# Optimization experiments

Hardware: AMD Instinct MI355X
Metric: run time of the kernel (lower is better)

Reference implementation:

```python
import jax, jax.numpy as jnp
import numpy as np

HEAD = 8

def _mvn(x, eps=1e-5):
    # per-(batch,channel) mean/std over spatial dims; torch .var default is unbiased (ddof=1)
    mean = jnp.mean(x, axis=(2, 3), keepdims=True)
    var = jnp.var(x, axis=(2, 3), ddof=1, keepdims=True) + eps
    return (x - mean) / jnp.sqrt(var)

def _conv1x1(x, w, b):
    return jnp.einsum('bchw,oc->bohw', x, w) + b[None, :, None, None]

def _block_heads(x, p):
    # non-overlapping unfold (kernel==stride==p): pure reshape; matches torch unfold ordering
    b, c, h, w = x.shape
    y = x.reshape(b, c, h // p, p, w // p, p).transpose(0, 1, 2, 4, 3, 5)
    n, r = (h // p) * (w // p), p * p
    return y.reshape(b, HEAD, c // HEAD, n, r)

def _unblock(x, p, h, w):
    # inverse of non-overlapping unfold (fold with kernel==stride)
    b, c, n, r = x.shape
    y = x.reshape(b, c, h // p, w // p, p, p).transpose(0, 1, 2, 4, 3, 5)
    return y.reshape(b, c, h, w)

def setup_inputs() -> dict:
    key = jax.random.key(0)
    ks = jax.random.split(key, 12)
    B, C, H, W = 4, 512, 64, 64
    wmat = lambda k: jax.random.normal(k, (C, C), jnp.float32) * 0.05
    zb = jnp.zeros((C,), jnp.float32)
    return {
        'content': jax.random.normal(ks[0], (B, C, H, W), jnp.float32),
        'style': jax.random.normal(ks[1], (B, C, H, W), jnp.float32),
        'q_w': wmat(ks[2]), 'q_b': zb,
        'k_w': wmat(ks[3]), 'k_b': zb,
        'v_w': wmat(ks[4]), 'v_b': zb,
        'q2_w': wmat(ks[5]), 'q2_b': zb,
        'k2_w': wmat(ks[6]), 'k2_b': zb,
        'v2_w': wmat(ks[7]), 'v2_b': zb,
        'f1_w': wmat(ks[8]), 'f1_b': zb,
        'f2_w': wmat(ks[9]), 'f2_b': zb,
        'sim_alpha': jnp.ones((1,), jnp.float32),
        'sim_beta': jnp.zeros((1,), jnp.float32),
        'layer': 3,
    }

def reference(content, style, q_w, q_b, k_w, k_b, v_w, v_b, q2_w, q2_b, k2_w, k2_b,
              v2_w, v2_b, f1_w, f1_b, f2_w, f2_b, sim_alpha, sim_beta, layer):
    region = 8 if int(layer) in (3, 4) else 4
    b, c, h, w = content.shape
    nc = _mvn(content)
    ns = _mvn(style)
    DA_q = _block_heads(_conv1x1(nc, q_w, q_b), region)      # [b,H,ch,n,r]
    DA_k = _block_heads(_conv1x1(ns, k_w, k_b), region)
    DA_v = _block_heads(_conv1x1(style, v_w, v_b), region)
    PA_q = _block_heads(_conv1x1(nc, q2_w, q2_b), region)
    PA_k = _block_heads(_conv1x1(ns, k2_w, k2_b), region)
    PA_v = _block_heads(_conv1x1(style, v2_w, v2_b), region)
    r = region * region
    n = DA_q.shape[3]
    # --- distinctiveness attention: mean-center clustering + sigmoid-weighted aggregation ---
    DA_k_c = jnp.mean(DA_k, axis=-1)                          # [b,H,ch,n]
    DA_v_c = jnp.mean(DA_v, axis=-1)
    dis = jnp.einsum('bhcx,bhcxy->bhxy', DA_k_c, DA_k)
    sim = jax.nn.sigmoid(sim_beta + sim_alpha * dis)          # [b,H,n,r]
    DA_k_agg = (jnp.einsum('bhxy,bhcxy->bhcx', sim, DA_k) + DA_k_c) / (r + 1)
    DA_v_agg = (jnp.einsum('bhxy,bhcxy->bhcx', sim, DA_v) + DA_v_c) / (r + 1)
    logits = jnp.einsum('bhcxy,bhcz->bhyxz', DA_q, DA_k_agg)  # [b,H,r,n,n]
    scores = jax.nn.softmax(logits, axis=-1)
    DA = jnp.einsum('bhyxz,bhcz->bhcxy', scores, DA_v_agg)    # [b,H,ch,n,r]
    DA_ub = _unblock(DA.reshape(b, c, n, r), region, h, w)
    # --- point attention: argmax NN block matching, then intra-block attention ---
    PA1 = jnp.einsum('bhcxy,bhczy->bhxz', PA_q, PA_k)         # [b,H,n,n]
    idx = jnp.argmax(PA1, axis=-1)                            # [b,H,n]
    idx_b = jnp.broadcast_to(idx[:, :, None, :, None], PA_k.shape)
    PA_k_rs = jnp.take_along_axis(PA_k, idx_b, axis=3)
    PA_v_rs = jnp.take_along_axis(PA_v, idx_b, axis=3)
    logits2 = jnp.einsum('bhcxy,bhcxz->bhxyz', PA_q, PA_k_rs) # [b,H,n,r,r]
    scores2 = jax.nn.softmax(logits2, axis=-1)
    PA = jnp.einsum('bhxyz,bhcxz->bhcxy', scores2, PA_v_rs)
    PA_ub = _unblock(PA.reshape(b, c, n, r), region, h, w)
    O = _conv1x1(DA_ub, f1_w, f1_b) + _conv1x1(PA_ub, f2_w, f2_b)
    return O + content
```

## Files before the change

kernel.cpp:

```cpp
#include <hip/hip_runtime.h>

typedef unsigned short u16;
typedef unsigned int   u32;
typedef _Float16       f16;

typedef f16   f16x8 __attribute__((ext_vector_type(8)));
typedef f16   f16x4 __attribute__((ext_vector_type(4)));
typedef float f32x4 __attribute__((ext_vector_type(4)));

__device__ __forceinline__ f32x4 mfma16(f16x8 a, f16x8 b, f32x4 c){
  return __builtin_amdgcn_mfma_f32_16x16x32_f16(a, b, c, 0, 0, 0);
}

__device__ __forceinline__ void glds16(const f16* g, f16* l){
  __builtin_amdgcn_global_load_lds(
      (const __attribute__((address_space(1))) void*)g,
      (__attribute__((address_space(3))) void*)l, 16, 0, 0);
}

__device__ __forceinline__ void barrier_f(){
  __builtin_amdgcn_s_barrier();
  asm volatile("" ::: "memory");
}

__global__ __launch_bounds__(256) void k_mvn_stats(
    const float* __restrict__ content, const float* __restrict__ style,
    float* __restrict__ stats)
{
  const int src = blockIdx.x >> 11;
  const int row = blockIdx.x & 2047;
  const float* xp = (src ? style : content) + (size_t)row * 4096;
  const int t = threadIdx.x;
  double s = 0.0, ss = 0.0;
  for(int i = t * 4; i < 4096; i += 1024){
    float4 v = *(const float4*)(xp + i);
    s  += (double)v.x + (double)v.y + (double)v.z + (double)v.w;
    ss += (double)v.x * v.x + (double)v.y * v.y + (double)v.z * v.z + (double)v.w * v.w;
  }
  #pragma unroll
  for(int off = 32; off > 0; off >>= 1){
    s  += __shfl_xor(s, off);
    ss += __shfl_xor(ss, off);
  }
  __shared__ double sh[8];
  const int wid = t >> 6;
  if((t & 63) == 0){ sh[wid] = s; sh[4 + wid] = ss; }
  __syncthreads();
  if(t == 0){
    double S  = sh[0] + sh[1] + sh[2] + sh[3];
    double SS = sh[4] + sh[5] + sh[6] + sh[7];
    float mean = (float)(S * (1.0 / 4096.0));
    float var  = (float)((SS - S * S * (1.0 / 4096.0)) * (1.0 / 4095.0));
    stats[src * 4096 + row] = mean;
    stats[src * 4096 + 2048 + row] = rsqrtf(var + 1e-5f);
  }
}

__global__ __launch_bounds__(256) void k_prep_w_all(
    const float* __restrict__ qW,  const float* __restrict__ qB,
    const float* __restrict__ kW,  const float* __restrict__ kB,
    const float* __restrict__ q2W, const float* __restrict__ q2B,
    const float* __restrict__ k2W, const float* __restrict__ k2B,
    const float* __restrict__ vW,  const float* __restrict__ vB,
    const float* __restrict__ v2W, const float* __restrict__ v2B,
    const float* __restrict__ f1W, const float* __restrict__ f2W,
    const float* __restrict__ stats,
    f16* __restrict__ qw, f16* __restrict__ kw,
    f16* __restrict__ q2wh, f16* __restrict__ q2wl,
    f16* __restrict__ k2wh, f16* __restrict__ k2wl,
    f16* __restrict__ vw, f16* __restrict__ v2w,
    f16* __restrict__ f1w, f16* __restrict__ f2w,
    float* __restrict__ biasp)
{
  const int t = threadIdx.x;
  int rid = blockIdx.x * 32 + (t >> 3);
  const float *W; const float *B = nullptr;
  int side = -1, b = 0, o;
  f16 *oh; f16 *ol = nullptr; float* bs = nullptr;
  if(rid < 2048){
    b = rid >> 9; o = rid & 511;
    W = qW; B = qB; side = 0;
    oh = qw + (size_t)(b * 512 + o) * 512;
    bs = biasp + 0 * 2048 + b * 512 + o;
  } else if(rid < 4096){
    rid -= 2048; b = rid >> 9; o = rid & 511;
    W = kW; B = kB; side = 1;
    oh = kw + (size_t)(b * 512 + o) * 512;
    bs = biasp + 1 * 2048 + b * 512 + o;
  } else if(rid < 6144){
    rid -= 4096; b = rid >> 9; o = rid & 511;
    W = q2W; B = q2B; side = 0;
    oh = q2wh + (size_t)(b * 512 + o) * 512;
    ol = q2wl + (size_t)(b * 512 + o) * 512;
    bs = biasp + 4 * 2048 + b * 512 + o;
  } else if(rid < 8192){
    rid -= 6144; b = rid >> 9; o = rid & 511;
    W = k2W; B = k2B; side = 1;
    oh = k2wh + (size_t)(b * 512 + o) * 512;
    ol = k2wl + (size_t)(b * 512 + o) * 512;
    bs = biasp + 5 * 2048 + b * 512 + o;
  } else if(rid < 8704){
    o = rid - 8192; W = vW; B = vB;
    oh = vw + (size_t)o * 512;
    bs = biasp + 2 * 2048 + o;
  } else if(rid < 9216){
    o = rid - 8704; W = v2W; B = v2B;
    oh = v2w + (size_t)o * 512;
    bs = biasp + 3 * 2048 + o;
  } else if(rid < 9728){
    o = rid - 9216; W = f1W;
    oh = f1w + (size_t)o * 512;
  } else {
    o = rid - 9728; W = f2W;
    oh = f2w + (size_t)o * 512;
  }
  const float* mp = (side >= 0) ? stats + side * 4096 + b * 512 : nullptr;
  const float* rp = (side >= 0) ? mp + 2048 : nullptr;
  const int c0 = (t & 7) * 64;
  float dot = 0.f;
  #pragma unroll
  for(int i = 0; i < 64; i += 8){
    int c = c0 + i;
    float w[8];
    *(float4*)(w)     = *(const float4*)(W + (size_t)o * 512 + c);
    *(float4*)(w + 4) = *(const float4*)(W + (size_t)o * 512 + c + 4);
    f16x8 h8, l8;
    #pragma unroll
    for(int j = 0; j < 8; j++){
      float wp = w[j];
      if(side >= 0){
        float r = rp[c + j];
        dot += wp * mp[c + j] * r;
        wp *= r;
      }
      f16 h = (f16)wp;
      h8[j] = h; l8[j] = (f16)(wp - (float)h);
    }
    *(f16x8*)(oh + c) = h8;
    if(ol) *(f16x8*)(ol + c) = l8;
  }
  if(bs){
    dot += __shfl_xor(dot, 1); dot += __shfl_xor(dot, 2); dot += __shfl_xor(dot, 4);
    if((t & 7) == 0) *bs = B[o] - dot;
  }
}

__global__ __launch_bounds__(256) void k_prep_x(
    const float* __restrict__ content, const float* __restrict__ style,
    f16* __restrict__ cth, f16* __restrict__ ctl,
    f16* __restrict__ sth, f16* __restrict__ stl)
{
  const int side = blockIdx.z;
  const int b = blockIdx.y;
  const int s0 = blockIdx.x * 128;
  const float* Xb = (side ? style : content) + (size_t)b * 512 * 4096;
  f16* Oh = (side ? sth : cth) + (size_t)b * 4096 * 512;
  f16* Ol = (side ? stl : ctl) + (size_t)b * 4096 * 512;
  __shared__ float Xs[32][132];
  const int t = threadIdx.x;
  const int s = t >> 1, half = t & 1;
  for(int cc = 0; cc < 512; cc += 32){
    __syncthreads();
    #pragma unroll
    for(int u = 0; u < 4; u++){
      int q = t + u * 256;
      int row = q >> 5, f4 = q & 31;
      float4 v = *(const float4*)(Xb + (size_t)(cc + row) * 4096 + s0 + f4 * 4);
      *(float4*)(&Xs[row][f4 * 4]) = v;
    }
    __syncthreads();
    f16x8 h0, h1, l0, l1;
    #pragma unroll
    for(int i = 0; i < 8; i++){
      float x = Xs[half * 16 + i][s];
      f16 h = (f16)x; h0[i] = h; l0[i] = (f16)(x - (float)h);
    }
    #pragma unroll
    for(int i = 0; i < 8; i++){
      float x = Xs[half * 16 + 8 + i][s];
      f16 h = (f16)x; h1[i] = h; l1[i] = (f16)(x - (float)h);
    }
    size_t o = (size_t)(s0 + s) * 512 + cc + half * 16;
    *(f16x8*)(Oh + o) = h0; *(f16x8*)(Oh + o + 8) = h1;
    *(f16x8*)(Ol + o) = l0; *(f16x8*)(Ol + o + 8) = l1;
  }
}

__global__ __launch_bounds__(256) void k_convT(
    const f16* __restrict__ Xt, const f16* __restrict__ Wp,
    const float* __restrict__ bias, int bw, f16* __restrict__ Out)
{
  const int b = blockIdx.z;
  const int o0 = blockIdx.y * 128;
  const int s0 = blockIdx.x * 128;
  const f16* Xb = Xt + (size_t)b * 4096 * 512;
  const f16* Wb = Wp + (bw ? (size_t)b * 262144 : 0);
  const float* bp = bias + (bw ? b * 512 : 0);
  f16* Ob = Out + (size_t)b * 512 * 4096;
  __shared__ f16 As[2][4096];
  __shared__ f16 Bs[2][4096];
  const int t = threadIdx.x;
  const int lane = t & 63, wid = t >> 6;
  const int wm = (wid >> 1) * 64, wn = (wid & 1) * 64;
  const int lr = lane & 15, lg = lane >> 4;
  const int sr = lane >> 2, sc = lane & 3;
  auto STAGE = [&](int d, int kk){
    #pragma unroll
    for(int i = 0; i < 2; i++){
      int r0 = wid * 32 + i * 16;
      int rr = r0 + sr;
      int cs = (sc ^ ((rr >> 1) & 3)) << 3;
      glds16(Wb + (size_t)(o0 + rr) * 512 + kk + cs, As[d] + r0 * 32);
      glds16(Xb + (size_t)(s0 + rr) * 512 + kk + cs, Bs[d] + r0 * 32);
    }
  };
  f32x4 acc[4][4] = {};
  STAGE(0, 0);
  int db = 0;
  for(int tt = 0; tt < 16; tt++){
    if(tt < 15){
      STAGE(db ^ 1, (tt + 1) * 32);
      asm volatile("s_waitcnt vmcnt(4)" ::: "memory");
    } else {
      asm volatile("s_waitcnt vmcnt(0)" ::: "memory");
    }
    barrier_f();
    f16x8 av[4], bv[4];
    #pragma unroll
    for(int mi = 0; mi < 4; mi++){
      int row = wm + mi * 16 + lr;
      av[mi] = *(const f16x8*)(As[db] + row * 32 + ((lg ^ ((row >> 1) & 3)) << 3));
    }
    #pragma unroll
    for(int ni = 0; ni < 4; ni++){
      int row = wn + ni * 16 + lr;
      bv[ni] = *(const f16x8*)(Bs[db] + row * 32 + ((lg ^ ((row >> 1) & 3)) << 3));
    }
    #pragma unroll
    for(int mi = 0; mi < 4; mi++){
      #pragma unroll
      for(int ni = 0; ni < 4; ni++)
        acc[mi][ni] = mfma16(av[mi], bv[ni], acc[mi][ni]);
    }
    barrier_f();
    db ^= 1;
  }
  #pragma unroll
  for(int mi = 0; mi < 4; mi++){
    #pragma unroll
    for(int ni = 0; ni < 4; ni++){
      #pragma unroll
      for(int j = 0; j < 4; j++){
        int o = o0 + wm + mi * 16 + lg * 4 + j;
        int s = s0 + wn + ni * 16 + lr;
        Ob[(size_t)o * 4096 + s] = (f16)(acc[mi][ni][j] + bp[o]);
      }
    }
  }
}

__global__ __launch_bounds__(256) void k_conv3out(
    const f16* __restrict__ Xt,
    const f16* __restrict__ Wk, const f16* __restrict__ Wv, const f16* __restrict__ Wv2,
    const float* __restrict__ biasp,
    f16* __restrict__ Ok, f16* __restrict__ Ov, f16* __restrict__ Ov2)
{
  const int b = blockIdx.z;
  const int seg = blockIdx.y >> 2;
  const int o0 = (blockIdx.y & 3) * 128;
  const int s0 = blockIdx.x * 128;
  const f16* Xb = Xt + (size_t)b * 4096 * 512;
  const f16* Wb = seg == 0 ? Wk + (size_t)b * 262144 : (seg == 1 ? Wv : Wv2);
  const float* bp = biasp + (seg == 0 ? 1 * 2048 + b * 512 : (seg == 1 ? 2 * 2048 : 3 * 2048));
  f16* Ob = (seg == 0 ? Ok : (seg == 1 ? Ov : Ov2)) + (size_t)b * 512 * 4096;
  __shared__ f16 As[2][4096];
  __shared__ f16 Bs[2][4096];
  const int t = threadIdx.x;
  const int lane = t & 63, wid = t >> 6;
  const int wm = (wid >> 1) * 64, wn = (wid & 1) * 64;
  const int lr = lane & 15, lg = lane >> 4;
  const int sr = lane >> 2, sc = lane & 3;
  auto STAGE = [&](int d, int kk){
    #pragma unroll
    for(int i = 0; i < 2; i++){
      int r0 = wid * 32 + i * 16;
      int rr = r0 + sr;
      int cs = (sc ^ ((rr >> 1) & 3)) << 3;
      glds16(Wb + (size_t)(o0 + rr) * 512 + kk + cs, As[d] + r0 * 32);
      glds16(Xb + (size_t)(s0 + rr) * 512 + kk + cs, Bs[d] + r0 * 32);
    }
  };
  f32x4 acc[4][4] = {};
  STAGE(0, 0);
  int db = 0;
  for(int tt = 0; tt < 16; tt++){
    if(tt < 15){
      STAGE(db ^ 1, (tt + 1) * 32);
      asm volatile("s_waitcnt vmcnt(4)" ::: "memory");
    } else {
      asm volatile("s_waitcnt vmcnt(0)" ::: "memory");
    }
    barrier_f();
    f16x8 av[4], bv[4];
    #pragma unroll
    for(int mi = 0; mi < 4; mi++){
      int row = wm + mi * 16 + lr;
      av[mi] = *(const f16x8*)(As[db] + row * 32 + ((lg ^ ((row >> 1) & 3)) << 3));
    }
    #pragma unroll
    for(int ni = 0; ni < 4; ni++){
      int row = wn + ni * 16 + lr;
      bv[ni] = *(const f16x8*)(Bs[db] + row * 32 + ((lg ^ ((row >> 1) & 3)) << 3));
    }
    #pragma unroll
    for(int mi = 0; mi < 4; mi++){
      #pragma unroll
      for(int ni = 0; ni < 4; ni++)
        acc[mi][ni] = mfma16(av[mi], bv[ni], acc[mi][ni]);
    }
    barrier_f();
    db ^= 1;
  }
  #pragma unroll
  for(int mi = 0; mi < 4; mi++){
    #pragma unroll
    for(int ni = 0; ni < 4; ni++){
      #pragma unroll
      for(int j = 0; j < 4; j++){
        int o = o0 + wm + mi * 16 + lg * 4 + j;
        int s = s0 + wn + ni * 16 + lr;
        Ob[(size_t)o * 4096 + s] = (f16)(acc[mi][ni][j] + bp[o]);
      }
    }
  }
}

__global__ __launch_bounds__(256) void k_pa1(
    const f16* __restrict__ Qh, const f16* __restrict__ Kh, float* __restrict__ pa1p)
{
  const int slice = blockIdx.x & 7;
  const int bh = blockIdx.x >> 3;
  const size_t base = (size_t)bh * 64 * 4096;
  __shared__ f16 Ah[2][64][72], Bh[2][64][72];
  const int t = threadIdx.x;
  const int lane = t & 63, wid = t >> 6;
  const int wm = (wid >> 1) * 32, wn = (wid & 1) * 32;
  const int lr = lane & 15, lg = lane >> 4;
  f32x4 acc[2][2] = {};
  for(int chunk = 0; chunk < 4; chunk++){
    const int c0 = slice * 8 + chunk * 2;
    __syncthreads();
    #pragma unroll
    for(int cc = 0; cc < 2; cc++){
      size_t cbase = base + (size_t)(c0 + cc) * 4096;
      #pragma unroll
      for(int u = 0; u < 2; u++){
        int e = u * 256 + t;
        int x = e >> 3, yh = e & 7;
        size_t src = cbase + (size_t)((x >> 3) * 512 + (x & 7) * 8 + yh * 64);
        int dst = yh * 8;
        *(f16x8*)(&Ah[cc][x][dst]) = *(const f16x8*)(Qh + src);
        *(f16x8*)(&Bh[cc][x][dst]) = *(const f16x8*)(Kh + src);
      }
    }
    __syncthreads();
    #pragma unroll
    for(int cc = 0; cc < 2; cc++){
      #pragma unroll
      for(int kc = 0; kc < 2; kc++){
        f16x8 ah[2], bh[2];
        #pragma unroll
        for(int mi = 0; mi < 2; mi++)
          ah[mi] = *(const f16x8*)(&Ah[cc][wm + mi * 16 + lr][kc * 32 + lg * 8]);
        #pragma unroll
        for(int ni = 0; ni < 2; ni++)
          bh[ni] = *(const f16x8*)(&Bh[cc][wn + ni * 16 + lr][kc * 32 + lg * 8]);
        #pragma unroll
        for(int mi = 0; mi < 2; mi++){
          #pragma unroll
          for(int ni = 0; ni < 2; ni++)
            acc[mi][ni] = mfma16(ah[mi], bh[ni], acc[mi][ni]);
        }
      }
    }
  }
  float* outp = pa1p + ((size_t)bh * 8 + slice) * 4096;
  #pragma unroll
  for(int mi = 0; mi < 2; mi++){
    #pragma unroll
    for(int ni = 0; ni < 2; ni++){
      #pragma unroll
      for(int j = 0; j < 4; j++){
        int x = wm + mi * 16 + lg * 4 + j;
        int z = wn + ni * 16 + lr;
        outp[x * 64 + z] = acc[mi][ni][j];
      }
    }
  }
}

__global__ __launch_bounds__(64) void k_pa1r(
    float* __restrict__ pa1p, int* __restrict__ idx, int* __restrict__ flags)
{
  const int bh = blockIdx.x;
  const int x = threadIdx.x;
  float* p = pa1p + (size_t)bh * 8 * 4096 + x * 64;
  float m1 = -3e38f, m2 = -3e38f; int i1 = 0;
  for(int z = 0; z < 64; z += 4){
    float4 v = *(const float4*)(p + z);
    #pragma unroll
    for(int sl = 1; sl < 8; sl++){
      float4 w = *(const float4*)(p + sl * 4096 + z);
      v.x += w.x; v.y += w.y; v.z += w.z; v.w += w.w;
    }
    *(float4*)(p + z) = v;
    float vv[4] = {v.x, v.y, v.z, v.w};
    #pragma unroll
    for(int k = 0; k < 4; k++){
      if(vv[k] > m1){ m2 = m1; m1 = vv[k]; i1 = z + k; }
      else if(vv[k] > m2){ m2 = vv[k]; }
    }
  }
  idx[bh * 64 + x] = i1;
  flags[bh * 64 + x] = (m2 >= m1 - 0.5f) ? 1 : 0;
}

__global__ __launch_bounds__(256) void k_refine(
    const f16* __restrict__ Xqh, const f16* __restrict__ Xql,
    const f16* __restrict__ Xkh, const f16* __restrict__ Xkl,
    const f16* __restrict__ Wqh, const f16* __restrict__ Wql,
    const f16* __restrict__ Wkh, const f16* __restrict__ Wkl,
    const float* __restrict__ biasp, const float* __restrict__ pa1p,
    const int* __restrict__ flags, int* __restrict__ idx)
{
  const int bid = blockIdx.x;
  if(flags[bid] == 0) return;
  const int bh = bid >> 6, x = bid & 63;
  const int b = bh >> 3, hd = bh & 7;
  __shared__ __align__(16) f16 Ah[64][72], Al[64][72], Bh[64][72], Bl[64][72];
  __shared__ float q2s[64][65];
  __shared__ float red[4];
  __shared__ float vals[64];
  __shared__ int cand[64];
  const int t = threadIdx.x;
  const int lane = t & 63, wid = t >> 6;
  const int wm = (wid >> 1) * 32, wn = (wid & 1) * 32;
  const int lr = lane & 15, lg = lane >> 4;
  const int srw = t >> 2, soc = (t & 3) * 2;

  auto gemm = [&](const f16* Wh_, const f16* Wl_, const f16* Xh_, const f16* Xl_,
                  int blk, f32x4 (&acc)[2][2]){
    const size_t wrow = ((size_t)(b * 512 + hd * 64 + srw)) * 512 + soc * 8;
    const int s = (blk >> 3) * 512 + (blk & 7) * 8 + (srw >> 3) * 64 + (srw & 7);
    const size_t xrow = ((size_t)b * 4096 + s) * 512 + soc * 8;
    f16x8 r0, r1, r2, r3, r4, r5, r6, r7;
    #define RLOAD(ch, a0,a1,a2,a3,a4,a5,a6,a7) do{            \
      a0 = *(const f16x8*)(Wh_ + wrow + (ch) * 64);           \
      a1 = *(const f16x8*)(Wh_ + wrow + (ch) * 64 + 8);       \
      a2 = *(const f16x8*)(Wl_ + wrow + (ch) * 64);           \
      a3 = *(const f16x8*)(Wl_ + wrow + (ch) * 64 + 8);       \
      a4 = *(const f16x8*)(Xh_ + xrow + (ch) * 64);           \
      a5 = *(const f16x8*)(Xh_ + xrow + (ch) * 64 + 8);       \
      a6 = *(const f16x8*)(Xl_ + xrow + (ch) * 64);           \
      a7 = *(const f16x8*)(Xl_ + xrow + (ch) * 64 + 8);       \
    }while(0)
    RLOAD(0, r0,r1,r2,r3,r4,r5,r6,r7);
    #pragma unroll
    for(int ch = 0; ch < 8; ch++){
      __syncthreads();
      *(f16x8*)(&Ah[srw][soc * 8])     = r0;
      *(f16x8*)(&Ah[srw][soc * 8 + 8]) = r1;
      *(f16x8*)(&Al[srw][soc * 8])     = r2;
      *(f16x8*)(&Al[srw][soc * 8 + 8]) = r3;
      *(f16x8*)(&Bh[srw][soc * 8])     = r4;
      *(f16x8*)(&Bh[srw][soc * 8 + 8]) = r5;
      *(f16x8*)(&Bl[srw][soc * 8])     = r6;
      *(f16x8*)(&Bl[srw][soc * 8 + 8]) = r7;
      f16x8 n0, n1, n2, n3, n4, n5, n6, n7;
      if(ch < 7) RLOAD(ch + 1, n0,n1,n2,n3,n4,n5,n6,n7);
// ... 283 lines not shown
    }
  }
}

__global__ __launch_bounds__(256) void k_pa2(
    const f16* __restrict__ Qh, const f16* __restrict__ Kh,
    const f16* __restrict__ V2, const int* __restrict__ idx, f16* __restrict__ OutT)
{
  const int hw = blockIdx.x;
  const int bh = (hw & 7) * 4 + ((hw >> 3) >> 6);
  const int x  = (hw >> 3) & 63;
  const int b_ = bh >> 3, hd = bh & 7;
  const size_t base = (size_t)bh * 64 * 4096;
  f16* Ot = OutT + (size_t)b_ * 4096 * 512 + hd * 64;

  __shared__ __align__(16) char Ubuf[18432];
  __shared__ f16 Vn[64][72];
  __shared__ f16 Ps[64][72];
  f16   (*Qt)[72] = (f16(*)[72])Ubuf;
  f16   (*Kt)[72] = (f16(*)[72])(Ubuf + 9216);
  float (*Lf)[66] = (float(*)[66])Ubuf;
  float (*Os)[67] = (float(*)[67])Ubuf;

  const int t = threadIdx.x;
  const int lane = t & 63, wid = t >> 6;
  const int wm = (wid >> 1) * 32, wn = (wid & 1) * 32;
  const int lr = lane & 15, lg = lane >> 4;

  const int xk = idx[bh * 64 + x];
  const int xb = (x >> 3) * 512 + (x & 7) * 8;
  const int kb = (xk >> 3) * 512 + (xk & 7) * 8;

  {
    const int c = t >> 2, q4 = t & 3;
    #pragma unroll
    for(int u = 0; u < 2; u++){
      int yh = q4 * 2 + u;
      f16x8 q8 = *(const f16x8*)(Qh + base + (size_t)c * 4096 + xb + yh * 64);
      f16x8 k8 = *(const f16x8*)(Kh + base + (size_t)c * 4096 + kb + yh * 64);
      f16x8 v8 = *(const f16x8*)(V2 + base + (size_t)c * 4096 + kb + yh * 64);
      int col = ((((c >> 3) ^ yh) & 7) << 3) + (c & 7);
      #pragma unroll
      for(int j = 0; j < 8; j++){
        Qt[yh * 8 + j][col] = q8[j];
        Kt[yh * 8 + j][col] = k8[j];
      }
      *(f16x8*)(&Vn[c][yh * 8]) = v8;
    }
  }
  __syncthreads();

  f32x4 acc[2][2] = {};
  #pragma unroll
  for(int kc = 0; kc < 2; kc++){
    f16x8 af[2], bf[2];
    #pragma unroll
    for(int mi = 0; mi < 2; mi++){
      int row = wm + mi * 16 + lr;
      af[mi] = *(const f16x8*)(&Qt[row][((((kc * 4 + lg) ^ (row >> 3)) & 7) << 3)]);
    }
    #pragma unroll
    for(int ni = 0; ni < 2; ni++){
      int row = wn + ni * 16 + lr;
      bf[ni] = *(const f16x8*)(&Kt[row][((((kc * 4 + lg) ^ (row >> 3)) & 7) << 3)]);
    }
    #pragma unroll
    for(int mi = 0; mi < 2; mi++){
      #pragma unroll
      for(int ni = 0; ni < 2; ni++)
        acc[mi][ni] = mfma16(af[mi], bf[ni], acc[mi][ni]);
    }
  }
  __syncthreads();
  #pragma unroll
  for(int mi = 0; mi < 2; mi++){
    #pragma unroll
    for(int ni = 0; ni < 2; ni++){
      #pragma unroll
      for(int j = 0; j < 4; j++)
        Lf[wm + mi * 16 + lg * 4 + j][wn + ni * 16 + lr] = acc[mi][ni][j];
    }
  }
  __syncthreads();

  {
    const int y = t >> 2, zp = t & 3;
    float l[16];
    #pragma unroll
    for(int i = 0; i < 16; i++) l[i] = Lf[y][zp * 16 + i];
    float m = l[0];
    #pragma unroll
    for(int i = 1; i < 16; i++) m = fmaxf(m, l[i]);
    m = fmaxf(m, __shfl_xor(m, 1)); m = fmaxf(m, __shfl_xor(m, 2));
    float sum = 0.f;
    #pragma unroll
    for(int i = 0; i < 16; i++){ l[i] = expf(l[i] - m); sum += l[i]; }
    sum += __shfl_xor(sum, 1); sum += __shfl_xor(sum, 2);
    float inv = 1.f / sum;
    f16x8 p0, p1;
    #pragma unroll
    for(int i = 0; i < 8; i++){ p0[i] = (f16)(l[i] * inv); p1[i] = (f16)(l[8 + i] * inv); }
    *(f16x8*)(&Ps[y][zp * 16]) = p0;
    *(f16x8*)(&Ps[y][zp * 16 + 8]) = p1;
  }
  __syncthreads();

  f32x4 acc2[2][2] = {};
  #pragma unroll
  for(int kc = 0; kc < 2; kc++){
    f16x8 af[2], bf[2];
    #pragma unroll
    for(int mi = 0; mi < 2; mi++)
      af[mi] = *(const f16x8*)(&Ps[wm + mi * 16 + lr][kc * 32 + lg * 8]);
    #pragma unroll
    for(int ni = 0; ni < 2; ni++)
      bf[ni] = *(const f16x8*)(&Vn[wn + ni * 16 + lr][kc * 32 + lg * 8]);
    #pragma unroll
    for(int mi = 0; mi < 2; mi++){
      #pragma unroll
      for(int ni = 0; ni < 2; ni++)
        acc2[mi][ni] = mfma16(af[mi], bf[ni], acc2[mi][ni]);
    }
  }
  #pragma unroll
  for(int mi = 0; mi < 2; mi++){
    #pragma unroll
    for(int ni = 0; ni < 2; ni++){
      #pragma unroll
      for(int j = 0; j < 4; j++)
        Os[wn + ni * 16 + lr][wm + mi * 16 + lg * 4 + j] = acc2[mi][ni][j];
    }
  }
  __syncthreads();

  {
    const int y = t >> 2, cq = (t & 3) * 16;
    size_t srow = (size_t)(xb + (y >> 3) * 64 + (y & 7)) * 512;
    f16x8 w0, w1;
    #pragma unroll
    for(int i = 0; i < 8; i++){ w0[i] = (f16)Os[cq + i][y]; w1[i] = (f16)Os[cq + 8 + i][y]; }
    *(f16x8*)(Ot + srow + cq) = w0;
    *(f16x8*)(Ot + srow + cq + 8) = w1;
  }
}

__global__ __launch_bounds__(256) void k_finalT(
    const f16* __restrict__ X1t, const f16* __restrict__ X2t,
    const f16* __restrict__ W1p, const f16* __restrict__ W2p,
    const float* __restrict__ B1, const float* __restrict__ B2,
    const float* __restrict__ content, float* __restrict__ out)
{
  const int b = blockIdx.z;
  const int o0 = blockIdx.y * 128;
  const int s0 = blockIdx.x * 128;
  __shared__ f16 As[2][4096];
  __shared__ f16 Bs[2][4096];
  const int t = threadIdx.x;
  const int lane = t & 63, wid = t >> 6;
  const int wm = (wid >> 1) * 64, wn = (wid & 1) * 64;
  const int lr = lane & 15, lg = lane >> 4;
  const int sr = lane >> 2, sc = lane & 3;
  const f16* Xp[2] = {X1t + (size_t)b * 4096 * 512, X2t + (size_t)b * 4096 * 512};
  const f16* Wq[2] = {W1p, W2p};
  auto STAGE = [&](int d, int tt){
    const f16* Xb = Xp[tt >> 4];
    const f16* Wb = Wq[tt >> 4];
    int kk = (tt & 15) * 32;
    #pragma unroll
    for(int i = 0; i < 2; i++){
      int r0 = wid * 32 + i * 16;
      int rr = r0 + sr;
      int cs = (sc ^ ((rr >> 1) & 3)) << 3;
      glds16(Wb + (size_t)(o0 + rr) * 512 + kk + cs, As[d] + r0 * 32);
      glds16(Xb + (size_t)(s0 + rr) * 512 + kk + cs, Bs[d] + r0 * 32);
    }
  };
  f32x4 acc[4][4] = {};
  STAGE(0, 0);
  int db = 0;
  for(int tt = 0; tt < 32; tt++){
    if(tt < 31){
      STAGE(db ^ 1, tt + 1);
      asm volatile("s_waitcnt vmcnt(4)" ::: "memory");
    } else {
      asm volatile("s_waitcnt vmcnt(0)" ::: "memory");
    }
    barrier_f();
    f16x8 av[4], bv[4];
    #pragma unroll
    for(int mi = 0; mi < 4; mi++){
      int row = wm + mi * 16 + lr;
      av[mi] = *(const f16x8*)(As[db] + row * 32 + ((lg ^ ((row >> 1) & 3)) << 3));
    }
    #pragma unroll
    for(int ni = 0; ni < 4; ni++){
      int row = wn + ni * 16 + lr;
      bv[ni] = *(const f16x8*)(Bs[db] + row * 32 + ((lg ^ ((row >> 1) & 3)) << 3));
    }
    #pragma unroll
    for(int mi = 0; mi < 4; mi++){
      #pragma unroll
      for(int ni = 0; ni < 4; ni++)
        acc[mi][ni] = mfma16(av[mi], bv[ni], acc[mi][ni]);
    }
    barrier_f();
    db ^= 1;
  }
  #pragma unroll
  for(int mi = 0; mi < 4; mi++){
    #pragma unroll
    for(int ni = 0; ni < 4; ni++){
      #pragma unroll
      for(int j = 0; j < 4; j++){
        int o = o0 + wm + mi * 16 + lg * 4 + j;
        int s = s0 + wn + ni * 16 + lr;
        size_t gi = ((size_t)b * 512 + o) * 4096 + s;
        out[gi] = acc[mi][ni][j] + B1[o] + B2[o] + content[gi];
      }
    }
  }
}

extern "C" void kernel_launch(void* const* d_in, const int* in_sizes, int n_in,
                              void* d_out, int out_size, void* d_ws, size_t ws_size,
                              hipStream_t stream) {
  (void)in_sizes; (void)n_in; (void)out_size; (void)ws_size;
  const float* content = (const float*)d_in[0];
  const float* style   = (const float*)d_in[1];
  const float* q_w  = (const float*)d_in[2];  const float* q_b  = (const float*)d_in[3];
  const float* k_w  = (const float*)d_in[4];  const float* k_b  = (const float*)d_in[5];
  const float* v_w  = (const float*)d_in[6];  const float* v_b  = (const float*)d_in[7];
  const float* q2_w = (const float*)d_in[8];  const float* q2_b = (const float*)d_in[9];
  const float* k2_w = (const float*)d_in[10]; const float* k2_b = (const float*)d_in[11];
  const float* v2_w = (const float*)d_in[12]; const float* v2_b = (const float*)d_in[13];
  const float* f1_w = (const float*)d_in[14]; const float* f1_b = (const float*)d_in[15];
  const float* f2_w = (const float*)d_in[16]; const float* f2_b = (const float*)d_in[17];
  const float* sim_alpha = (const float*)d_in[18];
  const float* sim_beta  = (const float*)d_in[19];

  char* ws = (char*)d_ws;
  #define SLOT(i) (ws + (size_t)(i) * 16777216)
  f16* cth = (f16*)SLOT(0);
  f16* ctl = (f16*)SLOT(1);
  f16* sth = (f16*)SLOT(2);
  f16* stl = (f16*)SLOT(3);
  f16* wbase = (f16*)SLOT(4);
  f16* qw   = wbase;
  f16* kw   = wbase + 1 * 1048576;
  f16* q2wh = wbase + 2 * 1048576;
  f16* q2wl = wbase + 3 * 1048576;
  f16* k2wh = wbase + 4 * 1048576;
  f16* k2wl = wbase + 5 * 1048576;
  f16* vw   = wbase + 6 * 1048576;
  f16* v2w  = vw + 262144;
  f16* f1w  = vw + 524288;
  f16* f2w  = vw + 786432;
  f16*   q2h   = (f16*)SLOT(5);
  f16*   k2h   = (f16*)SLOT(6);
  float* pa1p  = (float*)SLOT(7);
  int*   flags = (int*)(ws + 7 * 16777216 + 8388608);
  f16*   qbuf  = (f16*)SLOT(3);
  f16*   kbuf  = (f16*)SLOT(0);
  f16*   vbuf  = (f16*)SLOT(1);
  f16*   v2buf = (f16*)SLOT(7);
  f16*   da_t  = (f16*)SLOT(2);
  f16*   pa_t  = (f16*)SLOT(3);
  float* stats = (float*)(ws + 134217728);
  float* biasp = (float*)(ws + 134217728 + 32768);
  float* kagg  = (float*)(ws + 134217728 + 32768);
  float* vagg  = (float*)(ws + 134217728 + 557056);
  int*   idxb  = (int*)(ws + 134217728 + 1081344);

  dim3 gconv(32, 4, 4);

  k_mvn_stats<<<4096, 256, 0, stream>>>(content, style, stats);

  k_prep_w_all<<<320, 256, 0, stream>>>(
      q_w, q_b, k_w, k_b, q2_w, q2_b, k2_w, k2_b,
      v_w, v_b, v2_w, v2_b, f1_w, f2_w, stats,
      qw, kw, q2wh, q2wl, k2wh, k2wl, vw, v2w, f1w, f2w, biasp);

  k_prep_x<<<dim3(32,4,2), 256, 0, stream>>>(content, style, cth, ctl, sth, stl);

  k_convT<<<gconv, 256, 0, stream>>>(cth, q2wh, biasp + 4 * 2048, 1, q2h);
  k_convT<<<gconv, 256, 0, stream>>>(sth, k2wh, biasp + 5 * 2048, 1, k2h);
  k_pa1<<<256, 256, 0, stream>>>(q2h, k2h, pa1p);
  k_pa1r<<<32, 64, 0, stream>>>(pa1p, idxb, flags);
  k_refine<<<2048, 256, 0, stream>>>(cth, ctl, sth, stl,
                                     q2wh, q2wl, k2wh, k2wl,
                                     biasp, pa1p, flags, idxb);

  k_convT<<<gconv, 256, 0, stream>>>(cth, qw, biasp + 0 * 2048, 1, qbuf);
  k_conv3out<<<dim3(32,12,4), 256, 0, stream>>>(sth, kw, vw, v2w, biasp,
                                                kbuf, vbuf, v2buf);

  k_da1<<<2048, 256, 0, stream>>>(kbuf, vbuf, sim_alpha, sim_beta, kagg, vagg);
  k_da2<<<512, 256, 0, stream>>>(qbuf, kagg, vagg, da_t);
  k_pa2<<<2048, 256, 0, stream>>>(q2h, k2h, v2buf, idxb, pa_t);

  k_finalT<<<gconv, 256, 0, stream>>>(da_t, pa_t, f1w, f2w, f1_b, f2_b,
                                      content, (float*)d_out);
}
```

Baseline: 298.4 us.

## Fuse MVN statistics into input transpose and widen conv GEMM tiles

Drops the separate mean/variance kernel: k_prep_x now accumulates per-channel sum and sum of squares from its shared-memory tile into a zeroed stats buffer with float atomics, and k_prep_w_all derives mean and rsqrt from those sums. This saves one full read of content and style. Separately, the 1x1-conv GEMM kernels (convT, conv3out, finalT) double the spatial tile to 256, which halves the grid and doubles per-wave accumulators and LDS use. The costs are fp32 single-pass variance with atomics instead of double precision, which risks accuracy, plus higher register pressure and fewer blocks (256 for convT) on a large GPU.

```diff
diff --git a/kernel.cpp b/kernel.cpp
--- a/kernel.cpp
+++ b/kernel.cpp
@@ -21,39 +21,6 @@
 __device__ __forceinline__ void barrier_f(){
   __builtin_amdgcn_s_barrier();
   asm volatile("" ::: "memory");
-}
-
-__global__ __launch_bounds__(256) void k_mvn_stats(
-    const float* __restrict__ content, const float* __restrict__ style,
-    float* __restrict__ stats)
-{
-  const int src = blockIdx.x >> 11;
-  const int row = blockIdx.x & 2047;
-  const float* xp = (src ? style : content) + (size_t)row * 4096;
-  const int t = threadIdx.x;
-  double s = 0.0, ss = 0.0;
-  for(int i = t * 4; i < 4096; i += 1024){
-    float4 v = *(const float4*)(xp + i);
-    s  += (double)v.x + (double)v.y + (double)v.z + (double)v.w;
-    ss += (double)v.x * v.x + (double)v.y * v.y + (double)v.z * v.z + (double)v.w * v.w;
-  }
-  #pragma unroll
-  for(int off = 32; off > 0; off >>= 1){
-    s  += __shfl_xor(s, off);
-    ss += __shfl_xor(ss, off);
-  }
-  __shared__ double sh[8];
-  const int wid = t >> 6;
-  if((t & 63) == 0){ sh[wid] = s; sh[4 + wid] = ss; }
-  __syncthreads();
-  if(t == 0){
-    double S  = sh[0] + sh[1] + sh[2] + sh[3];
-    double SS = sh[4] + sh[5] + sh[6] + sh[7];
-    float mean = (float)(S * (1.0 / 4096.0));
-    float var  = (float)((SS - S * S * (1.0 / 4096.0)) * (1.0 / 4095.0));
-    stats[src * 4096 + row] = mean;
-    stats[src * 4096 + 2048 + row] = rsqrtf(var + 1e-5f);
-  }
 }
 
 __global__ __launch_bounds__(256) void k_prep_w_all(
@@ -114,8 +81,8 @@
     o = rid - 9728; W = f2W;
     oh = f2w + (size_t)o * 512;
   }
-  const float* mp = (side >= 0) ? stats + side * 4096 + b * 512 : nullptr;
-  const float* rp = (side >= 0) ? mp + 2048 : nullptr;
+  const float* Sv  = (side >= 0) ? stats + side * 4096 + b * 512 : nullptr;
+  const float* SSv = Sv ? Sv + 2048 : nullptr;
   const int c0 = (t & 7) * 64;
   float dot = 0.f;
   #pragma unroll
@@ -129,8 +96,10 @@
     for(int j = 0; j < 8; j++){
       float wp = w[j];
       if(side >= 0){
-        float r = rp[c + j];
-        dot += wp * mp[c + j] * r;
+        float S = Sv[c + j], SS = SSv[c + j];
+        float mean = S * (1.f / 4096.f);
+        float r = rsqrtf((SS - S * mean) * (1.f / 4095.f) + 1e-5f);
+        dot += wp * mean * r;
         wp *= r;
       }
       f16 h = (f16)wp;
@@ -148,7 +117,8 @@
 __global__ __launch_bounds__(256) void k_prep_x(
     const float* __restrict__ content, const float* __restrict__ style,
     f16* __restrict__ cth, f16* __restrict__ ctl,
-    f16* __restrict__ sth, f16* __restrict__ stl)
+    f16* __restrict__ sth, f16* __restrict__ stl,
+    float* __restrict__ stats)
 {
   const int side = blockIdx.z;
   const int b = blockIdx.y;
@@ -156,6 +126,7 @@
   const float* Xb = (side ? style : content) + (size_t)b * 512 * 4096;
   f16* Oh = (side ? sth : cth) + (size_t)b * 4096 * 512;
   f16* Ol = (side ? stl : ctl) + (size_t)b * 4096 * 512;
+  float* Sg = stats + side * 4096 + b * 512;
   __shared__ float Xs[32][132];
   const int t = threadIdx.x;
   const int s = t >> 1, half = t & 1;
@@ -183,6 +154,21 @@
     size_t o = (size_t)(s0 + s) * 512 + cc + half * 16;
     *(f16x8*)(Oh + o) = h0; *(f16x8*)(Oh + o + 8) = h1;
     *(f16x8*)(Ol + o) = l0; *(f16x8*)(Ol + o + 8) = l1;
+    {
+      const int cl = t >> 3, part = t & 7;
+      float s1 = 0.f, s2 = 0.f;
+      #pragma unroll
+      for(int i = 0; i < 16; i++){
+        float xv = Xs[cl][part * 16 + i];
+        s1 += xv; s2 += xv * xv;
+      }
+      s1 += __shfl_xor(s1, 1); s1 += __shfl_xor(s1, 2); s1 += __shfl_xor(s1, 4);
+      s2 += __shfl_xor(s2, 1); s2 += __shfl_xor(s2, 2); s2 += __shfl_xor(s2, 4);
+      if(part == 0){
+        atomicAdd(Sg + cc + cl, s1);
+        atomicAdd(Sg + 2048 + cc + cl, s2);
+      }
+    }
   }
 }
 
@@ -192,16 +178,16 @@
 {
   const int b = blockIdx.z;
   const int o0 = blockIdx.y * 128;
-  const int s0 = blockIdx.x * 128;
+  const int s0 = blockIdx.x * 256;
   const f16* Xb = Xt + (size_t)b * 4096 * 512;
   const f16* Wb = Wp + (bw ? (size_t)b * 262144 : 0);
   const float* bp = bias + (bw ? b * 512 : 0);
   f16* Ob = Out + (size_t)b * 512 * 4096;
   __shared__ f16 As[2][4096];
-  __shared__ f16 Bs[2][4096];
+  __shared__ f16 Bs[2][8192];
   const int t = threadIdx.x;
   const int lane = t & 63, wid = t >> 6;
-  const int wm = (wid >> 1) * 64, wn = (wid & 1) * 64;
+  const int wm = (wid >> 1) * 64, wn = (wid & 1) * 128;
   const int lr = lane & 15, lg = lane >> 4;
   const int sr = lane >> 2, sc = lane & 3;
   auto STAGE = [&](int d, int kk){
@@ -211,35 +197,41 @@
       int rr = r0 + sr;
       int cs = (sc ^ ((rr >> 1) & 3)) << 3;
       glds16(Wb + (size_t)(o0 + rr) * 512 + kk + cs, As[d] + r0 * 32);
+    }
+    #pragma unroll
+    for(int i = 0; i < 4; i++){
+      int r0 = wid * 64 + i * 16;
+      int rr = r0 + sr;
+      int cs = (sc ^ ((rr >> 1) & 3)) << 3;
       glds16(Xb + (size_t)(s0 + rr) * 512 + kk + cs, Bs[d] + r0 * 32);
     }
   };
-  f32x4 acc[4][4] = {};
+  f32x4 acc[4][8] = {};
   STAGE(0, 0);
   int db = 0;
   for(int tt = 0; tt < 16; tt++){
     if(tt < 15){
       STAGE(db ^ 1, (tt + 1) * 32);
-      asm volatile("s_waitcnt vmcnt(4)" ::: "memory");
+      asm volatile("s_waitcnt vmcnt(6)" ::: "memory");
     } else {
       asm volatile("s_waitcnt vmcnt(0)" ::: "memory");
     }
     barrier_f();
-    f16x8 av[4], bv[4];
+    f16x8 av[4], bv[8];
     #pragma unroll
     for(int mi = 0; mi < 4; mi++){
       int row = wm + mi * 16 + lr;
       av[mi] = *(const f16x8*)(As[db] + row * 32 + ((lg ^ ((row >> 1) & 3)) << 3));
     }
     #pragma unroll
-    for(int ni = 0; ni < 4; ni++){
+    for(int ni = 0; ni < 8; ni++){
       int row = wn + ni * 16 + lr;
       bv[ni] = *(const f16x8*)(Bs[db] + row * 32 + ((lg ^ ((row >> 1) & 3)) << 3));
     }
     #pragma unroll
     for(int mi = 0; mi < 4; mi++){
       #pragma unroll
-      for(int ni = 0; ni < 4; ni++)
+      for(int ni = 0; ni < 8; ni++)
         acc[mi][ni] = mfma16(av[mi], bv[ni], acc[mi][ni]);
     }
     barrier_f();
@@ -248,7 +240,7 @@
   #pragma unroll
   for(int mi = 0; mi < 4; mi++){
     #pragma unroll
-    for(int ni = 0; ni < 4; ni++){
+    for(int ni = 0; ni < 8; ni++){
       #pragma unroll
       for(int j = 0; j < 4; j++){
         int o = o0 + wm + mi * 16 + lg * 4 + j;
@@ -268,16 +260,16 @@
   const int b = blockIdx.z;
   const int seg = blockIdx.y >> 2;
   const int o0 = (blockIdx.y & 3) * 128;
-  const int s0 = blockIdx.x * 128;
+  const int s0 = blockIdx.x * 256;
   const f16* Xb = Xt + (size_t)b * 4096 * 512;
   const f16* Wb = seg == 0 ? Wk + (size_t)b * 262144 : (seg == 1 ? Wv : Wv2);
   const float* bp = biasp + (seg == 0 ? 1 * 2048 + b * 512 : (seg == 1 ? 2 * 2048 : 3 * 2048));
   f16* Ob = (seg == 0 ? Ok : (seg == 1 ? Ov : Ov2)) + (size_t)b * 512 * 4096;
   __shared__ f16 As[2][4096];
-  __shared__ f16 Bs[2][4096];
+  __shared__ f16 Bs[2][8192];
   const int t = threadIdx.x;
   const int lane = t & 63, wid = t >> 6;
-  const int wm = (wid >> 1) * 64, wn = (wid & 1) * 64;
+  const int wm = (wid >> 1) * 64, wn = (wid & 1) * 128;
   const int lr = lane & 15, lg = lane >> 4;
   const int sr = lane >> 2, sc = lane & 3;
   auto STAGE = [&](int d, int kk){
@@ -287,35 +279,41 @@
       int rr = r0 + sr;
       int cs = (sc ^ ((rr >> 1) & 3)) << 3;
       glds16(Wb + (size_t)(o0 + rr) * 512 + kk + cs, As[d] + r0 * 32);
+    }
+    #pragma unroll
+    for(int i = 0; i < 4; i++){
+      int r0 = wid * 64 + i * 16;
+      int rr = r0 + sr;
+      int cs = (sc ^ ((rr >> 1) & 3)) << 3;
       glds16(Xb + (size_t)(s0 + rr) * 512 + kk + cs, Bs[d] + r0 * 32);
     }
   };
-  f32x4 acc[4][4] = {};
+  f32x4 acc[4][8] = {};
   STAGE(0, 0);
   int db = 0;
   for(int tt = 0; tt < 16; tt++){
     if(tt < 15){
       STAGE(db ^ 1, (tt + 1) * 32);
-      asm volatile("s_waitcnt vmcnt(4)" ::: "memory");
+      asm volatile("s_waitcnt vmcnt(6)" ::: "memory");
     } else {
       asm volatile("s_waitcnt vmcnt(0)" ::: "memory");
     }
     barrier_f();
-    f16x8 av[4], bv[4];
+    f16x8 av[4], bv[8];
     #pragma unroll
     for(int mi = 0; mi < 4; mi++){
       int row = wm + mi * 16 + lr;
       av[mi] = *(const f16x8*)(As[db] + row * 32 + ((lg ^ ((row >> 1) & 3)) << 3));
     }
     #pragma unroll
-    for(int ni = 0; ni < 4; ni++){
+    for(int ni = 0; ni < 8; ni++){
       int row = wn + ni * 16 + lr;
       bv[ni] = *(const f16x8*)(Bs[db] + row * 32 + ((lg ^ ((row >> 1) & 3)) << 3));
     }
     #pragma unroll
     for(int mi = 0; mi < 4; mi++){
       #pragma unroll
-      for(int ni = 0; ni < 4; ni++)
+      for(int ni = 0; ni < 8; ni++)
         acc[mi][ni] = mfma16(av[mi], bv[ni], acc[mi][ni]);
     }
     barrier_f();
@@ -324,7 +322,7 @@
   #pragma unroll
   for(int mi = 0; mi < 4; mi++){
     #pragma unroll
-    for(int ni = 0; ni < 4; ni++){
+    for(int ni = 0; ni < 8; ni++){
       #pragma unroll
       for(int j = 0; j < 4; j++){
         int o = o0 + wm + mi * 16 + lg * 4 + j;
@@ -914,12 +912,12 @@
 {
   const int b = blockIdx.z;
   const int o0 = blockIdx.y * 128;
-  const int s0 = blockIdx.x * 128;
+  const int s0 = blockIdx.x * 256;
   __shared__ f16 As[2][4096];
-  __shared__ f16 Bs[2][4096];
+  __shared__ f16 Bs[2][8192];
   const int t = threadIdx.x;
   const int lane = t & 63, wid = t >> 6;
-  const int wm = (wid >> 1) * 64, wn = (wid & 1) * 64;
+  const int wm = (wid >> 1) * 64, wn = (wid & 1) * 128;
   const int lr = lane & 15, lg = lane >> 4;
   const int sr = lane >> 2, sc = lane & 3;
   const f16* Xp[2] = {X1t + (size_t)b * 4096 * 512, X2t + (size_t)b * 4096 * 512};
@@ -934,35 +932,41 @@
       int rr = r0 + sr;
       int cs = (sc ^ ((rr >> 1) & 3)) << 3;
       glds16(Wb + (size_t)(o0 + rr) * 512 + kk + cs, As[d] + r0 * 32);
+    }
+    #pragma unroll
+    for(int i = 0; i < 4; i++){
+      int r0 = wid * 64 + i * 16;
+      int rr = r0 + sr;
+      int cs = (sc ^ ((rr >> 1) & 3)) << 3;
       glds16(Xb + (size_t)(s0 + rr) * 512 + kk + cs, Bs[d] + r0 * 32);
     }
   };
-  f32x4 acc[4][4] = {};
+  f32x4 acc[4][8] = {};
   STAGE(0, 0);
   int db = 0;
   for(int tt = 0; tt < 32; tt++){
     if(tt < 31){
       STAGE(db ^ 1, tt + 1);
-      asm volatile("s_waitcnt vmcnt(4)" ::: "memory");
+      asm volatile("s_waitcnt vmcnt(6)" ::: "memory");
     } else {
       asm volatile("s_waitcnt vmcnt(0)" ::: "memory");
     }
     barrier_f();
-    f16x8 av[4], bv[4];
+    f16x8 av[4], bv[8];
     #pragma unroll
     for(int mi = 0; mi < 4; mi++){
       int row = wm + mi * 16 + lr;
       av[mi] = *(const f16x8*)(As[db] + row * 32 + ((lg ^ ((row >> 1) & 3)) << 3));
     }
     #pragma unroll
-    for(int ni = 0; ni < 4; ni++){
+    for(int ni = 0; ni < 8; ni++){
       int row = wn + ni * 16 + lr;
       bv[ni] = *(const f16x8*)(Bs[db] + row * 32 + ((lg ^ ((row >> 1) & 3)) << 3));
     }
     #pragma unroll
     for(int mi = 0; mi < 4; mi++){
       #pragma unroll
-      for(int ni = 0; ni < 4; ni++)
+      for(int ni = 0; ni < 8; ni++)
         acc[mi][ni] = mfma16(av[mi], bv[ni], acc[mi][ni]);
     }
     barrier_f();
@@ -971,7 +975,7 @@
   #pragma unroll
   for(int mi = 0; mi < 4; mi++){
     #pragma unroll
-    for(int ni = 0; ni < 4; ni++){
+    for(int ni = 0; ni < 8; ni++){
       #pragma unroll
       for(int j = 0; j < 4; j++){
         int o = o0 + wm + mi * 16 + lg * 4 + j;
@@ -1033,16 +1037,16 @@
   float* vagg  = (float*)(ws + 134217728 + 557056);
   int*   idxb  = (int*)(ws + 134217728 + 1081344);
 
-  dim3 gconv(32, 4, 4);
-
-  k_mvn_stats<<<4096, 256, 0, stream>>>(content, style, stats);
+  dim3 gconv(16, 4, 4);
+
+  hipMemsetAsync(stats, 0, 32768, stream);
+
+  k_prep_x<<<dim3(32,4,2), 256, 0, stream>>>(content, style, cth, ctl, sth, stl, stats);
 
   k_prep_w_all<<<320, 256, 0, stream>>>(
       q_w, q_b, k_w, k_b, q2_w, q2_b, k2_w, k2_b,
       v_w, v_b, v2_w, v2_b, f1_w, f2_w, stats,
       qw, kw, q2wh, q2wl, k2wh, k2wl, vw, v2w, f1w, f2w, biasp);
-
-  k_prep_x<<<dim3(32,4,2), 256, 0, stream>>>(content, style, cth, ctl, sth, stl);
 
   k_convT<<<gconv, 256, 0, stream>>>(cth, q2wh, biasp + 4 * 2048, 1, q2h);
   k_convT<<<gconv, 256, 0, stream>>>(sth, k2wh, biasp + 5 * 2048, 1, k2h);
@@ -1053,7 +1057,7 @@
                                      biasp, pa1p, flags, idxb);
 
   k_convT<<<gconv, 256, 0, stream>>>(cth, qw, biasp + 0 * 2048, 1, qbuf);
-  k_conv3out<<<dim3(32,12,4), 256, 0, stream>>>(sth, kw, vw, v2w, biasp,
+  k_conv3out<<<dim3(16,12,4), 256, 0, stream>>>(sth, kw, vw, v2w, biasp,
                                                 kbuf, vbuf, v2buf);
 
   k_da1<<<2048, 256, 0, stream>>>(kbuf, vbuf, sim_alpha, sim_beta, kagg, vagg);
```

Measured after the change: 337.8 us. 1.13x slower.

## Fuse MVN statistics into input conversion kernel with atomic partial sums

Applied to the files above, without the earlier changes.

Removes the separate per-channel mean/variance kernel, which reread both 32MB inputs, and instead accumulates sum and sum-of-squares in the transposing f16 conversion kernel using atomics into a zeroed buffer. The weight-prep kernel now derives mean and rsqrt(var) from those raw sums. This saves one full pass over the inputs but switches from double to float accumulation with a one-pass variance formula, which risks precision loss, and adds a memset and atomic traffic.

```diff
diff --git a/kernel.cpp b/kernel.cpp
--- a/kernel.cpp
+++ b/kernel.cpp
@@ -21,39 +21,6 @@
 __device__ __forceinline__ void barrier_f(){
   __builtin_amdgcn_s_barrier();
   asm volatile("" ::: "memory");
-}
-
-__global__ __launch_bounds__(256) void k_mvn_stats(
-    const float* __restrict__ content, const float* __restrict__ style,
-    float* __restrict__ stats)
-{
-  const int src = blockIdx.x >> 11;
-  const int row = blockIdx.x & 2047;
-  const float* xp = (src ? style : content) + (size_t)row * 4096;
-  const int t = threadIdx.x;
-  double s = 0.0, ss = 0.0;
-  for(int i = t * 4; i < 4096; i += 1024){
-    float4 v = *(const float4*)(xp + i);
-    s  += (double)v.x + (double)v.y + (double)v.z + (double)v.w;
-    ss += (double)v.x * v.x + (double)v.y * v.y + (double)v.z * v.z + (double)v.w * v.w;
-  }
-  #pragma unroll
-  for(int off = 32; off > 0; off >>= 1){
-    s  += __shfl_xor(s, off);
-    ss += __shfl_xor(ss, off);
-  }
-  __shared__ double sh[8];
-  const int wid = t >> 6;
-  if((t & 63) == 0){ sh[wid] = s; sh[4 + wid] = ss; }
-  __syncthreads();
-  if(t == 0){
-    double S  = sh[0] + sh[1] + sh[2] + sh[3];
-    double SS = sh[4] + sh[5] + sh[6] + sh[7];
-    float mean = (float)(S * (1.0 / 4096.0));
-    float var  = (float)((SS - S * S * (1.0 / 4096.0)) * (1.0 / 4095.0));
-    stats[src * 4096 + row] = mean;
-    stats[src * 4096 + 2048 + row] = rsqrtf(var + 1e-5f);
-  }
 }
 
 __global__ __launch_bounds__(256) void k_prep_w_all(
@@ -114,8 +81,8 @@
     o = rid - 9728; W = f2W;
     oh = f2w + (size_t)o * 512;
   }
-  const float* mp = (side >= 0) ? stats + side * 4096 + b * 512 : nullptr;
-  const float* rp = (side >= 0) ? mp + 2048 : nullptr;
+  const float* Sv  = (side >= 0) ? stats + side * 4096 + b * 512 : nullptr;
+  const float* SSv = Sv ? Sv + 2048 : nullptr;
   const int c0 = (t & 7) * 64;
   float dot = 0.f;
   #pragma unroll
@@ -129,8 +96,10 @@
     for(int j = 0; j < 8; j++){
       float wp = w[j];
       if(side >= 0){
-        float r = rp[c + j];
-        dot += wp * mp[c + j] * r;
+        float S = Sv[c + j], SS = SSv[c + j];
+        float mean = S * (1.f / 4096.f);
+        float r = rsqrtf((SS - S * mean) * (1.f / 4095.f) + 1e-5f);
+        dot += wp * mean * r;
         wp *= r;
       }
       f16 h = (f16)wp;
@@ -148,7 +117,8 @@
 __global__ __launch_bounds__(256) void k_prep_x(
     const float* __restrict__ content, const float* __restrict__ style,
     f16* __restrict__ cth, f16* __restrict__ ctl,
-    f16* __restrict__ sth, f16* __restrict__ stl)
+    f16* __restrict__ sth, f16* __restrict__ stl,
+    float* __restrict__ stats)
 {
   const int side = blockIdx.z;
   const int b = blockIdx.y;
@@ -156,6 +126,7 @@
   const float* Xb = (side ? style : content) + (size_t)b * 512 * 4096;
   f16* Oh = (side ? sth : cth) + (size_t)b * 4096 * 512;
   f16* Ol = (side ? stl : ctl) + (size_t)b * 4096 * 512;
+  float* Sg = stats + side * 4096 + b * 512;
   __shared__ float Xs[32][132];
   const int t = threadIdx.x;
   const int s = t >> 1, half = t & 1;
@@ -183,6 +154,21 @@
     size_t o = (size_t)(s0 + s) * 512 + cc + half * 16;
     *(f16x8*)(Oh + o) = h0; *(f16x8*)(Oh + o + 8) = h1;
     *(f16x8*)(Ol + o) = l0; *(f16x8*)(Ol + o + 8) = l1;
+    {
+      const int cl = t >> 3, part = t & 7;
+      float s1 = 0.f, s2 = 0.f;
+      #pragma unroll
+      for(int i = 0; i < 16; i++){
+        float xv = Xs[cl][part * 16 + i];
+        s1 += xv; s2 += xv * xv;
+      }
+      s1 += __shfl_xor(s1, 1); s1 += __shfl_xor(s1, 2); s1 += __shfl_xor(s1, 4);
+      s2 += __shfl_xor(s2, 1); s2 += __shfl_xor(s2, 2); s2 += __shfl_xor(s2, 4);
+      if(part == 0){
+        atomicAdd(Sg + cc + cl, s1);
+        atomicAdd(Sg + 2048 + cc + cl, s2);
+      }
+    }
   }
 }
 
@@ -1035,14 +1021,14 @@
 
   dim3 gconv(32, 4, 4);
 
-  k_mvn_stats<<<4096, 256, 0, stream>>>(content, style, stats);
+  hipMemsetAsync(stats, 0, 32768, stream);
+
+  k_prep_x<<<dim3(32,4,2), 256, 0, stream>>>(content, style, cth, ctl, sth, stl, stats);
 
   k_prep_w_all<<<320, 256, 0, stream>>>(
       q_w, q_b, k_w, k_b, q2_w, q2_b, k2_w, k2_b,
       v_w, v_b, v2_w, v2_b, f1_w, f2_w, stats,
       qw, kw, q2wh, q2wl, k2wh, k2wl, vw, v2w, f1w, f2w, biasp);
-
-  k_prep_x<<<dim3(32,4,2), 256, 0, stream>>>(content, style, cth, ctl, sth, stl);
 
   k_convT<<<gconv, 256, 0, stream>>>(cth, q2wh, biasp + 4 * 2048, 1, q2h);
   k_convT<<<gconv, 256, 0, stream>>>(sth, k2wh, biasp + 5 * 2048, 1, k2h);
```

Measured after the change: 304.6 us. 2.1% more time.
